# Kernel tuning notes

Measured on AMD Instinct MI355X. Metric: run time of the kernel, lower is better.

Reference implementation:

```python
import jax, jax.numpy as jnp
import numpy as np
from jax import lax

K = 4
H = 1024
IN = 512
OUT = 8192
T = 128
B = 32


def setup_inputs() -> dict:
    key = jax.random.key(0)
    ks = jax.random.split(key, 5)
    return {
        "X": jax.random.normal(ks[0], (T, B, IN), dtype=jnp.float32),
        "Wxh_w": jax.random.normal(ks[1], (H, IN), dtype=jnp.float32) * 0.02,
        "Wxh_b": jax.random.normal(ks[2], (H,), dtype=jnp.float32) * 0.02,
        "Whh_w": jax.random.normal(ks[3], (H, (K - 1) * H), dtype=jnp.float32) * 0.02,
        "Wmo_w": jax.random.normal(ks[4], (OUT, K * H), dtype=jnp.float32) * 0.02,
    }


def reference(X, Wxh_w, Wxh_b, Whh_w, Wmo_w):
    batch = X.shape[1]
    # history stack hs: [K-1, B, H], hs[0] = oldest, hs[-1] = newest
    hs0 = jnp.zeros((K - 1, batch, H), dtype=X.dtype)

    def step(hs, x_t):
        # concat reversed(h_prevs): newest block first -> [B, (K-1)*H]
        h_cat = hs[::-1].transpose(1, 0, 2).reshape(batch, (K - 1) * H)
        h_t = jax.nn.selu(x_t @ Wxh_w.T + Wxh_b + h_cat @ Whh_w.T)  # [B, H]
        h_out = jnp.concatenate([h_t, h_cat], axis=1)  # [B, K*H]
        out_t = h_out @ Wmo_w.T  # [B, OUT]
        new_hs = jnp.concatenate([hs[1:], h_t[None]], axis=0)
        # truncated BPTT: detach the (new) oldest hidden
        new_hs = new_hs.at[0].set(lax.stop_gradient(new_hs[0]))
        return new_hs, out_t

    _, outs = lax.scan(step, hs0, X)
    return outs  # [T, B, OUT]
```

## Files before the change

kernel.cpp:

```cpp
#include <hip/hip_runtime.h>
#include <hip/hip_bf16.h>

#define T_STEPS 128
#define BATCH   32
#define IN_DIM  512
#define H_DIM   1024
#define OUT_DIM 8192
#define KH      3072
#define NWG     128
#define SLOT_E  32768
#define NSLOT   131

typedef __attribute__((ext_vector_type(8))) short short8;
typedef __attribute__((ext_vector_type(4))) float f32x4;

__device__ __forceinline__ unsigned short bf16_rne(float f) {
  unsigned u = __float_as_uint(f);
  unsigned r = (u + 0x7FFFu + ((u >> 16) & 1u)) >> 16;
  return (unsigned short)r;
}

__device__ __forceinline__ void gload_lds16(const void* g, void* l) {
  __builtin_amdgcn_global_load_lds(
      (const __attribute__((address_space(1))) void*)g,
      (__attribute__((address_space(3))) void*)l, 16, 0, 0);
}

__global__ __launch_bounds__(256) void convert_kernel(
    const float* __restrict__ src, unsigned short* __restrict__ dst, int n4) {
  int i = blockIdx.x * blockDim.x + threadIdx.x;
  const int stride = gridDim.x * blockDim.x;
  for (; i < n4; i += stride) {
    float4 v = ((const float4*)src)[i];
    ushort4 o;
    o.x = bf16_rne(v.x); o.y = bf16_rne(v.y);
    o.z = bf16_rne(v.z); o.w = bf16_rne(v.w);
    ((ushort4*)dst)[i] = o;
  }
}

__global__ __launch_bounds__(256) void pre_kernel(
    const float* __restrict__ X, const float* __restrict__ Wxh,
    const float* __restrict__ bias, float* __restrict__ preT) {
  __shared__ float xs[32][260];
  const int tid = threadIdx.x;
  const int t  = blockIdx.x >> 4;
  const int jb = blockIdx.x & 15;
  const int b  = tid & 31;
  const int jg = tid >> 5;
  float acc[8];
  #pragma unroll
  for (int i = 0; i < 8; ++i) acc[i] = 0.f;

  for (int kc = 0; kc < 2; ++kc) {
    __syncthreads();
    #pragma unroll
    for (int v = tid; v < 2048; v += 256) {
      int br = v >> 6, i4 = v & 63;
      float4 x4 = *(const float4*)(X + (size_t)t*(BATCH*IN_DIM) + (size_t)br*IN_DIM + kc*256 + i4*4);
      *(float4*)&xs[br][i4*4] = x4;
    }
    __syncthreads();
    for (int i = 0; i < 256; i += 4) {
      const int k = kc*256 + i;
      float4 xv = *(const float4*)&xs[b][i];
      #pragma unroll
      for (int jj = 0; jj < 8; ++jj) {
        const int j = jb*64 + jg + jj*8;
        float4 w4 = *(const float4*)(Wxh + (size_t)j*IN_DIM + k);
        acc[jj] += xv.x*w4.x + xv.y*w4.y + xv.z*w4.z + xv.w*w4.w;
      }
    }
  }
  #pragma unroll
  for (int jj = 0; jj < 8; ++jj) {
    const int j = jb*64 + jg + jj*8;
    preT[(size_t)t*(H_DIM*BATCH) + (size_t)j*BATCH + b] = acc[jj] + bias[j];
  }
}

template<int RN, int RD1, int RD2>
__device__ __forceinline__ void do_step(
    const int t, const int tid, const int wg, const int j0,
    const int lane, const int wv,
    const short8* __restrict__ wf, const short8* __restrict__ hi8,
    const short8* __restrict__ lo8, const float* __restrict__ preT,
    unsigned short* __restrict__ hHi, unsigned short* __restrict__ hLo,
    int* __restrict__ grp, int* __restrict__ rootcnt, int* __restrict__ rootrep,
    short8 (&Rh0)[3][4], short8 (&Rh1)[3][4],
    short8 (&Rl0)[3][4], short8 (&Rl1)[3][4],
    float (&red)[8][16][33],
    unsigned short (&hpk_hi)[32][8], unsigned short (&hpk_lo)[32][8]) {
  f32x4 a0h = {}, a0l = {}, a1h = {}, a1l = {};

  #pragma unroll
  for (int i = 0; i < 4; ++i) {
    const int ks = 32 + wv*4 + i;
    const short8 af = wf[ks*64 + lane];
    a0h = __builtin_amdgcn_mfma_f32_16x16x32_bf16(af, Rh0[RD1][i], a0h, 0, 0, 0);
    a1h = __builtin_amdgcn_mfma_f32_16x16x32_bf16(af, Rh1[RD1][i], a1h, 0, 0, 0);
    a0l = __builtin_amdgcn_mfma_f32_16x16x32_bf16(af, Rl0[RD1][i], a0l, 0, 0, 0);
    a1l = __builtin_amdgcn_mfma_f32_16x16x32_bf16(af, Rl1[RD1][i], a1l, 0, 0, 0);
  }
  #pragma unroll
  for (int i = 0; i < 4; ++i) {
    const int ks = 64 + wv*4 + i;
    const short8 af = wf[ks*64 + lane];
    a0h = __builtin_amdgcn_mfma_f32_16x16x32_bf16(af, Rh0[RD2][i], a0h, 0, 0, 0);
    a1h = __builtin_amdgcn_mfma_f32_16x16x32_bf16(af, Rh1[RD2][i], a1h, 0, 0, 0);
    a0l = __builtin_amdgcn_mfma_f32_16x16x32_bf16(af, Rl0[RD2][i], a0l, 0, 0, 0);
    a1l = __builtin_amdgcn_mfma_f32_16x16x32_bf16(af, Rl1[RD2][i], a1l, 0, 0, 0);
  }

  float upre = 0.f;
  if (tid < 256)
    upre = preT[(size_t)t*(H_DIM*BATCH) + (size_t)(j0 + (tid >> 5))*BATCH + (tid & 31)];

  if (t > 0) {
    if (tid == 0) {
      while (!__hip_atomic_load(&rootrep[(((t-1) << 3) + (wg & 7)) << 4],
                                __ATOMIC_RELAXED, __HIP_MEMORY_SCOPE_AGENT))
        __builtin_amdgcn_s_sleep(2);
    }
    __syncthreads();
    asm volatile("" ::: "memory");
  }

  {
    const size_t sb = (size_t)(128 - t) * 4096;
    #pragma unroll
    for (int i = 0; i < 4; ++i) {
      const int ks = wv*4 + i;
      const size_t bidx = sb + (size_t)ks*128 + (size_t)(lane >> 4)*32 + (lane & 15);
      Rh0[RN][i] = hi8[bidx];
      Rh1[RN][i] = hi8[bidx + 16];
      Rl0[RN][i] = lo8[bidx];
      Rl1[RN][i] = lo8[bidx + 16];
    }
  }
  #pragma unroll
  for (int i = 0; i < 4; ++i) {
    const int ks = wv*4 + i;
    const short8 af = wf[ks*64 + lane];
    a0h = __builtin_amdgcn_mfma_f32_16x16x32_bf16(af, Rh0[RN][i], a0h, 0, 0, 0);
    a1h = __builtin_amdgcn_mfma_f32_16x16x32_bf16(af, Rh1[RN][i], a1h, 0, 0, 0);
    a0l = __builtin_amdgcn_mfma_f32_16x16x32_bf16(af, Rl0[RN][i], a0l, 0, 0, 0);
    a1l = __builtin_amdgcn_mfma_f32_16x16x32_bf16(af, Rl1[RN][i], a1l, 0, 0, 0);
  }

  const f32x4 s0 = a0h + a0l;
  const f32x4 s1 = a1h + a1l;
  const int rr = (lane >> 4) * 4, cc = lane & 15;
  #pragma unroll
  for (int q = 0; q < 4; ++q) {
    red[wv][rr + q][cc]      = s0[q];
    red[wv][rr + q][16 + cc] = s1[q];
  }
  __syncthreads();

  if (tid < 256) {
    const int jj = tid >> 5, b = tid & 31;
    float u = upre;
    #pragma unroll
    for (int w = 0; w < 8; ++w)
      u += red[w][jj][b] + red[w][jj + 8][b];
    const float h = u > 0.f ? 1.0507009873554805f*u
                            : (1.0507009873554805f*1.6732632423543772f)*expm1f(u);
    const unsigned short hh = bf16_rne(h);
    hpk_hi[b][jj] = hh;
    hpk_lo[b][jj] = bf16_rne(h - __uint_as_float((unsigned)hh << 16));
  }
  __syncthreads();

  if (tid < 32) {
    const int b = tid;
    const size_t base = (size_t)(127 - t)*SLOT_E + (size_t)(j0 >> 3)*256 + (size_t)b*8;
    const unsigned long long h0 = *(const unsigned long long*)&hpk_hi[b][0];
    const unsigned long long h1 = *(const unsigned long long*)&hpk_hi[b][4];
    const unsigned long long l0 = *(const unsigned long long*)&hpk_lo[b][0];
    const unsigned long long l1 = *(const unsigned long long*)&hpk_lo[b][4];
    __hip_atomic_store((unsigned long long*)(hHi + base),     h0, __ATOMIC_RELAXED, __HIP_MEMORY_SCOPE_AGENT);
    __hip_atomic_store((unsigned long long*)(hHi + base) + 1, h1, __ATOMIC_RELAXED, __HIP_MEMORY_SCOPE_AGENT);
    __hip_atomic_store((unsigned long long*)(hLo + base),     l0, __ATOMIC_RELAXED, __HIP_MEMORY_SCOPE_AGENT);
    __hip_atomic_store((unsigned long long*)(hLo + base) + 1, l1, __ATOMIC_RELAXED, __HIP_MEMORY_SCOPE_AGENT);
    if (t < T_STEPS - 1) {
      asm volatile("s_waitcnt vmcnt(0)" ::: "memory");
      if (tid == 0) {
        const int g = wg >> 3;
        if (__hip_atomic_fetch_add(&grp[((t << 4) + g) << 4], 1, __ATOMIC_RELAXED, __HIP_MEMORY_SCOPE_AGENT) == 7) {
          if (__hip_atomic_fetch_add(&rootcnt[t << 4], 1, __ATOMIC_RELAXED, __HIP_MEMORY_SCOPE_AGENT) == 15) {
            #pragma unroll
            for (int r = 0; r < 8; ++r)
              __hip_atomic_store(&rootrep[((t << 3) + r) << 4], 1,
                                 __ATOMIC_RELAXED, __HIP_MEMORY_SCOPE_AGENT);
          }
        }
      }
    }
  }
}

__global__ __launch_bounds__(512, 2) void recur_kernel(
    const float* __restrict__ Whh, const float* __restrict__ preT,
    unsigned short* __restrict__ hHi, unsigned short* __restrict__ hLo,
    int* __restrict__ grp, int* __restrict__ rootcnt, int* __restrict__ rootrep) {
  __shared__ __align__(16) unsigned short w_lds[96*64*8];
  __shared__ float red[8][16][33];
  __shared__ __align__(16) unsigned short hpk_hi[32][8];
  __shared__ __align__(16) unsigned short hpk_lo[32][8];
  const int tid  = threadIdx.x;
  const int wg   = blockIdx.x;
  const int j0   = wg * 8;
  const int lane = tid & 63;
  const int wv   = tid >> 6;

  for (int s = tid; s < 6144; s += 512) {
    const int ks = s >> 6, l = s & 63;
    const int r = l & 15;
    const int j = j0 + (r & 7);
    const int part = r >> 3;
    const int kb = ks*32 + (l >> 4)*8;
    const float* wp = Whh + (size_t)j*KH + kb;
    unsigned short tmp[8];
    #pragma unroll
    for (int i = 0; i < 8; ++i) {
      const float f = wp[i];
      unsigned short v = bf16_rne(f);
      if (part) v = bf16_rne(f - __uint_as_float((unsigned)v << 16));
      tmp[i] = v;
    }
    *(short8*)&w_lds[s*8] = *(short8*)tmp;
  }
  __syncthreads();

  const short8* wf  = (const short8*)w_lds;
  const short8* hi8 = (const short8*)hHi;
  const short8* lo8 = (const short8*)hLo;

  short8 Rh0[3][4], Rh1[3][4], Rl0[3][4], Rl1[3][4];
  const short8 z8 = {};
  #pragma unroll
  for (int r = 1; r < 3; ++r)
    #pragma unroll
    for (int i = 0; i < 4; ++i) {
      Rh0[r][i] = z8; Rh1[r][i] = z8; Rl0[r][i] = z8; Rl1[r][i] = z8;
    }

  for (int t3 = 0; t3 < 126; t3 += 3) {
    do_step<0,2,1>(t3,   tid, wg, j0, lane, wv, wf, hi8, lo8, preT, hHi, hLo,
                   grp, rootcnt, rootrep, Rh0, Rh1, Rl0, Rl1, red, hpk_hi, hpk_lo);
    do_step<1,0,2>(t3+1, tid, wg, j0, lane, wv, wf, hi8, lo8, preT, hHi, hLo,
                   grp, rootcnt, rootrep, Rh0, Rh1, Rl0, Rl1, red, hpk_hi, hpk_lo);
    do_step<2,1,0>(t3+2, tid, wg, j0, lane, wv, wf, hi8, lo8, preT, hHi, hLo,
                   grp, rootcnt, rootrep, Rh0, Rh1, Rl0, Rl1, red, hpk_hi, hpk_lo);
  }
  do_step<0,2,1>(126, tid, wg, j0, lane, wv, wf, hi8, lo8, preT, hHi, hLo,
                 grp, rootcnt, rootrep, Rh0, Rh1, Rl0, Rl1, red, hpk_hi, hpk_lo);
  do_step<1,0,2>(127, tid, wg, j0, lane, wv, wf, hi8, lo8, preT, hHi, hLo,
                 grp, rootcnt, rootrep, Rh0, Rh1, Rl0, Rl1, red, hpk_hi, hpk_lo);
}

__global__ __launch_bounds__(256) void gemm_kernel(
    const unsigned short* __restrict__ Ah, const unsigned short* __restrict__ Bm,
    float* __restrict__ C) {
  __shared__ __align__(16) unsigned short lA[2][4096];
  __shared__ __align__(16) unsigned short lB[2][4096];
  const int tid = threadIdx.x;
  const int wg = blockIdx.x;
  const int mb = wg & 31;
  const int nb = wg >> 5;
  const int lane = tid & 63;
  const int wv = tid >> 6;
  const int wm = wv >> 1, wn = wv & 1;
  const int lrow = lane & 15, lhalf = lane >> 4;
  const int rowB0 = tid >> 2, qB = tid & 3;
  f32x4 acc[4][4] = {};

#define STAGE(buf, kt) do {                                                    \
    _Pragma("unroll")                                                          \
    for (int it = 0; it < 2; ++it) {                                           \
      const int idxA = it*4 + wv;                                              \
      const int tA = mb*4 + (idxA >> 1);                                       \
      gload_lds16(Ah + (size_t)(127 - tA)*SLOT_E + (size_t)(kt)*1024           \
                     + (idxA & 1)*512 + (size_t)lane*8,                        \
                  &lA[buf][idxA*512]);                                         \
      const int rB = it*64 + rowB0;                                            \
      const int qs = qB ^ ((rB ^ (rB >> 2)) & 3);                              \
      gload_lds16(Bm + (size_t)(nb*128 + rB)*4096 + (size_t)(kt)*32 + qs*8,    \
                  &lB[buf][(tid & 192)*8 + it*2048]);                          \
    } } while (0)

  STAGE(0, 0);
  for (int kt = 0; kt < 128; ++kt) {
    const int cur = kt & 1;
    if (kt < 127) {
      STAGE(cur ^ 1, kt + 1);
      asm volatile("s_waitcnt vmcnt(4)" ::: "memory");
    } else {
      asm volatile("s_waitcnt vmcnt(0)" ::: "memory");
    }
    __syncthreads();
    short8 af[4], bf[4];
    #pragma unroll
    for (int mi = 0; mi < 4; ++mi) {
      const int tg = wm*2 + (mi >> 1);
      af[mi] = *(const short8*)&lA[cur][tg*1024 + lhalf*256 + (lrow + (mi & 1)*16)*8];
    }
    #pragma unroll
    for (int ni = 0; ni < 4; ++ni) {
      const int r = wn*64 + ni*16 + lrow;
      const int qs = lhalf ^ ((r ^ (r >> 2)) & 3);
      bf[ni] = *(const short8*)&lB[cur][r*32 + qs*8];
    }
    #pragma unroll
    for (int mi = 0; mi < 4; ++mi)
      #pragma unroll
      for (int ni = 0; ni < 4; ++ni)
        acc[mi][ni] = __builtin_amdgcn_mfma_f32_16x16x32_bf16(af[mi], bf[ni], acc[mi][ni], 0, 0, 0);
    __syncthreads();
  }
#undef STAGE

  const int orow0 = mb*128 + wm*64 + lhalf*4;
  const int ocol0 = nb*128 + wn*64 + lrow;
  #pragma unroll
  for (int mi = 0; mi < 4; ++mi)
    #pragma unroll
    for (int ni = 0; ni < 4; ++ni)
      #pragma unroll
      for (int q = 0; q < 4; ++q)
        __builtin_nontemporal_store(acc[mi][ni][q],
            &C[(size_t)(orow0 + mi*16 + q)*OUT_DIM + ocol0 + ni*16]);
}

extern "C" void kernel_launch(void* const* d_in, const int* in_sizes, int n_in,
                              void* d_out, int out_size, void* d_ws, size_t ws_size,
                              hipStream_t stream) {
  (void)in_sizes; (void)n_in; (void)out_size; (void)ws_size;
  const float* X   = (const float*)d_in[0];
  const float* Wxh = (const float*)d_in[1];
  const float* Wxb = (const float*)d_in[2];
  const float* Whh = (const float*)d_in[3];
  const float* Wmo = (const float*)d_in[4];
  float* out = (float*)d_out;
  char* ws = (char*)d_ws;

  const size_t OFF_PRET = 0;
  const size_t OFF_HHI  = OFF_PRET + (size_t)T_STEPS*H_DIM*BATCH*4;
  const size_t OFF_HLO  = OFF_HHI + (size_t)NSLOT*SLOT_E*2;
  const size_t OFF_GRP  = OFF_HLO + (size_t)NSLOT*SLOT_E*2;
  const size_t OFF_RCNT = OFF_GRP + (size_t)T_STEPS*16*64;
  const size_t OFF_RREP = OFF_RCNT + (size_t)T_STEPS*64;
  const size_t OFF_W16  = OFF_RREP + (size_t)T_STEPS*8*64;

  float* preT = (float*)(ws + OFF_PRET);
  unsigned short* hHi = (unsigned short*)(ws + OFF_HHI);
  unsigned short* hLo = (unsigned short*)(ws + OFF_HLO);
  int* grp     = (int*)(ws + OFF_GRP);
  int* rootcnt = (int*)(ws + OFF_RCNT);
  int* rootrep = (int*)(ws + OFF_RREP);
  unsigned short* Wmo16 = (unsigned short*)(ws + OFF_W16);

  hipMemsetAsync(hHi + (size_t)128*SLOT_E, 0, (size_t)3*SLOT_E*2, stream);
  hipMemsetAsync(hLo + (size_t)128*SLOT_E, 0, (size_t)3*SLOT_E*2, stream);
  hipMemsetAsync(grp, 0, (size_t)T_STEPS*16*64 + (size_t)T_STEPS*64
                        + (size_t)T_STEPS*8*64, stream);

  convert_kernel<<<2048, 256, 0, stream>>>(Wmo, Wmo16, (int)((size_t)OUT_DIM*4096/4));
  pre_kernel<<<2048, 256, 0, stream>>>(X, Wxh, Wxb, preT);
  recur_kernel<<<NWG, 512, 0, stream>>>(Whh, preT, hHi, hLo, grp, rootcnt, rootrep);
  gemm_kernel<<<2048, 256, 0, stream>>>(hHi, Wmo16, out);
}
```

Before: 1.138 ms.

## Replace output GEMM with 256x256-tile, 8-wave, 8-phase pipelined kernel

Rewrites the final output GEMM. It now uses 256x256 output tiles per workgroup with 512 threads, 128 KB of dynamic LDS holding double-buffered 64-wide K slices, and an eight-phase schedule that interleaves quarter-tile global-to-LDS staging with MFMA work. It also adds s_setprio around the MFMA bursts and a grouped block-to-tile mapping. The aim is to raise arithmetic intensity and overlap loads with compute. The cost is higher register and LDS pressure, and a fragile hand-written barrier and vmcnt schedule.

```diff
diff --git a/kernel.cpp b/kernel.cpp
--- a/kernel.cpp
+++ b/kernel.cpp
@@ -260,77 +260,121 @@
                  grp, rootcnt, rootrep, Rh0, Rh1, Rl0, Rl1, red, hpk_hi, hpk_lo);
 }
 
-__global__ __launch_bounds__(256) void gemm_kernel(
+__global__ __launch_bounds__(512, 2) void gemm256_kernel(
     const unsigned short* __restrict__ Ah, const unsigned short* __restrict__ Bm,
     float* __restrict__ C) {
-  __shared__ __align__(16) unsigned short lA[2][4096];
-  __shared__ __align__(16) unsigned short lB[2][4096];
+  extern __shared__ char smem[];
   const int tid = threadIdx.x;
   const int wg = blockIdx.x;
-  const int mb = wg & 31;
-  const int nb = wg >> 5;
+  const int x = wg & 7;
+  const int c = wg >> 3;
+  const int mb = c & 15;
+  const int nb = x*4 + (c >> 4);
   const int lane = tid & 63;
   const int wv = tid >> 6;
-  const int wm = wv >> 1, wn = wv & 1;
+  const int wm = wv >> 2;
+  const int wn = wv & 3;
   const int lrow = lane & 15, lhalf = lane >> 4;
-  const int rowB0 = tid >> 2, qB = tid & 3;
-  f32x4 acc[4][4] = {};
-
-#define STAGE(buf, kt) do {                                                    \
+  const int srow = tid & 127;
+  const int ss0 = tid >> 7;
+  int tA[2], bA[2];
+  #pragma unroll
+  for (int h = 0; h < 2; ++h) {
+    const int m = mb*256 + h*128 + srow;
+    tA[h] = m >> 5; bA[h] = m & 31;
+  }
+
+#define STAGE_A(HALF, BUF, KT) do {                                            \
     _Pragma("unroll")                                                          \
-    for (int it = 0; it < 2; ++it) {                                           \
-      const int idxA = it*4 + wv;                                              \
-      const int tA = mb*4 + (idxA >> 1);                                       \
-      gload_lds16(Ah + (size_t)(127 - tA)*SLOT_E + (size_t)(kt)*1024           \
-                     + (idxA & 1)*512 + (size_t)lane*8,                        \
-                  &lA[buf][idxA*512]);                                         \
-      const int rB = it*64 + rowB0;                                            \
-      const int qs = qB ^ ((rB ^ (rB >> 2)) & 3);                              \
-      gload_lds16(Bm + (size_t)(nb*128 + rB)*4096 + (size_t)(kt)*32 + qs*8,    \
-                  &lB[buf][(tid & 192)*8 + it*2048]);                          \
+    for (int u = 0; u < 2; ++u) {                                              \
+      const int s_ = u*4 + ss0;                                                \
+      gload_lds16(Ah + (size_t)(127 - tA[HALF])*SLOT_E                         \
+                     + (size_t)((KT)*8 + s_)*256 + bA[HALF]*8,                 \
+                  smem + (BUF)*65536 + (HALF)*16384 + u*8192 + tid*16);        \
     } } while (0)
 
-  STAGE(0, 0);
-  for (int kt = 0; kt < 128; ++kt) {
-    const int cur = kt & 1;
-    if (kt < 127) {
-      STAGE(cur ^ 1, kt + 1);
-      asm volatile("s_waitcnt vmcnt(4)" ::: "memory");
-    } else {
-      asm volatile("s_waitcnt vmcnt(0)" ::: "memory");
-    }
-    __syncthreads();
-    short8 af[4], bf[4];
-    #pragma unroll
-    for (int mi = 0; mi < 4; ++mi) {
-      const int tg = wm*2 + (mi >> 1);
-      af[mi] = *(const short8*)&lA[cur][tg*1024 + lhalf*256 + (lrow + (mi & 1)*16)*8];
-    }
-    #pragma unroll
-    for (int ni = 0; ni < 4; ++ni) {
-      const int r = wn*64 + ni*16 + lrow;
-      const int qs = lhalf ^ ((r ^ (r >> 2)) & 3);
-      bf[ni] = *(const short8*)&lB[cur][r*32 + qs*8];
-    }
-    #pragma unroll
-    for (int mi = 0; mi < 4; ++mi)
-      #pragma unroll
-      for (int ni = 0; ni < 4; ++ni)
-        acc[mi][ni] = __builtin_amdgcn_mfma_f32_16x16x32_bf16(af[mi], bf[ni], acc[mi][ni], 0, 0, 0);
-    __syncthreads();
-  }
-#undef STAGE
-
-  const int orow0 = mb*128 + wm*64 + lhalf*4;
-  const int ocol0 = nb*128 + wn*64 + lrow;
-  #pragma unroll
-  for (int mi = 0; mi < 4; ++mi)
-    #pragma unroll
-    for (int ni = 0; ni < 4; ++ni)
+#define STAGE_B(HALF, BUF, KT) do {                                            \
+    _Pragma("unroll")                                                          \
+    for (int u = 0; u < 2; ++u) {                                              \
+      const int s_ = u*4 + ss0;                                                \
+      gload_lds16(Bm + (size_t)(nb*256 + (HALF)*128 + srow)*4096               \
+                     + (size_t)(KT)*64 + s_*8,                                 \
+                  smem + (BUF)*65536 + 32768 + (HALF)*16384 + u*8192 + tid*16);\
+    } } while (0)
+
+  short8 aF[4][2], bF[2][2];
+  f32x4 acc[8][4] = {};
+
+#define PHASE(BUF, MH, NH, RDA, RDB, STAGE_STMT, DO_VM) do {                   \
+    if (RDA) {                                                                 \
+      _Pragma("unroll")                                                        \
+      for (int mi = 0; mi < 4; ++mi)                                           \
+        _Pragma("unroll")                                                      \
+        for (int kk = 0; kk < 2; ++kk)                                         \
+          aF[mi][kk] = *(const short8*)(smem + (BUF)*65536 + wm*16384          \
+              + (kk*4 + lhalf)*2048 + ((MH)*64 + mi*16 + lrow)*16);            \
+    }                                                                          \
+    if (RDB) {                                                                 \
+      _Pragma("unroll")                                                        \
+      for (int ni = 0; ni < 2; ++ni)                                           \
+        _Pragma("unroll")                                                      \
+        for (int kk = 0; kk < 2; ++kk)                                         \
+          bF[ni][kk] = *(const short8*)(smem + (BUF)*65536 + 32768             \
+              + (wn >> 1)*16384 + (kk*4 + lhalf)*2048                          \
+              + ((wn & 1)*64 + (NH)*32 + ni*16 + lrow)*16);                    \
+    }                                                                          \
+    STAGE_STMT;                                                                \
+    __builtin_amdgcn_s_barrier();                                              \
+    __builtin_amdgcn_s_setprio(1);                                             \
+    _Pragma("unroll")                                                          \
+    for (int mi = 0; mi < 4; ++mi)                                             \
+      _Pragma("unroll")                                                        \
+      for (int ni = 0; ni < 2; ++ni) {                                         \
+        acc[(MH)*4+mi][(NH)*2+ni] = __builtin_amdgcn_mfma_f32_16x16x32_bf16(   \
+            aF[mi][0], bF[ni][0], acc[(MH)*4+mi][(NH)*2+ni], 0, 0, 0);         \
+        acc[(MH)*4+mi][(NH)*2+ni] = __builtin_amdgcn_mfma_f32_16x16x32_bf16(   \
+            aF[mi][1], bF[ni][1], acc[(MH)*4+mi][(NH)*2+ni], 0, 0, 0);         \
+      }                                                                        \
+    __builtin_amdgcn_s_setprio(0);                                             \
+    if (DO_VM) asm volatile("s_waitcnt vmcnt(2)" ::: "memory");                \
+    __builtin_amdgcn_s_barrier();                                              \
+  } while (0)
+
+  STAGE_A(0, 0, 0);
+  STAGE_B(0, 0, 0);
+  STAGE_B(1, 0, 0);
+  STAGE_A(1, 0, 0);
+  STAGE_A(0, 1, 1);
+  asm volatile("s_waitcnt vmcnt(2)" ::: "memory");
+  __builtin_amdgcn_s_barrier();
+
+  for (int j = 0; j < 32; ++j) {
+    const int k1 = 2*j + 1;
+    const int k2 = (2*j + 2 < 64) ? 2*j + 2 : 63;
+    const int k3 = (2*j + 3 < 64) ? 2*j + 3 : 63;
+    PHASE(0, 0, 0, 1, 1, STAGE_B(0, 1, k1), 0);
+    PHASE(0, 0, 1, 0, 1, STAGE_B(1, 1, k1), 0);
+    PHASE(0, 1, 1, 1, 0, STAGE_A(1, 1, k1), 0);
+    PHASE(0, 1, 0, 0, 1, STAGE_A(0, 0, k2), 1);
+    PHASE(1, 0, 0, 1, 1, STAGE_B(0, 0, k2), 0);
+    PHASE(1, 0, 1, 0, 1, STAGE_B(1, 0, k2), 0);
+    PHASE(1, 1, 1, 1, 0, STAGE_A(1, 0, k2), 0);
+    PHASE(1, 1, 0, 0, 1, STAGE_A(0, 1, k3), 1);
+  }
+#undef PHASE
+#undef STAGE_A
+#undef STAGE_B
+
+  const int orow0 = mb*256 + wm*128 + lhalf*4;
+  const int ocol0 = nb*256 + wn*64 + lrow;
+  #pragma unroll
+  for (int m_ = 0; m_ < 8; ++m_)
+    #pragma unroll
+    for (int n_ = 0; n_ < 4; ++n_)
       #pragma unroll
       for (int q = 0; q < 4; ++q)
-        __builtin_nontemporal_store(acc[mi][ni][q],
-            &C[(size_t)(orow0 + mi*16 + q)*OUT_DIM + ocol0 + ni*16]);
+        __builtin_nontemporal_store(acc[m_][n_][q],
+            &C[(size_t)(orow0 + m_*16 + q)*OUT_DIM + ocol0 + n_*16]);
 }
 
 extern "C" void kernel_launch(void* const* d_in, const int* in_sizes, int n_in,
@@ -361,6 +405,9 @@
   int* rootrep = (int*)(ws + OFF_RREP);
   unsigned short* Wmo16 = (unsigned short*)(ws + OFF_W16);
 
+  (void)hipFuncSetAttribute(reinterpret_cast<const void*>(gemm256_kernel),
+                            hipFuncAttributeMaxDynamicSharedMemorySize, 131072);
+
   hipMemsetAsync(hHi + (size_t)128*SLOT_E, 0, (size_t)3*SLOT_E*2, stream);
   hipMemsetAsync(hLo + (size_t)128*SLOT_E, 0, (size_t)3*SLOT_E*2, stream);
   hipMemsetAsync(grp, 0, (size_t)T_STEPS*16*64 + (size_t)T_STEPS*64
@@ -369,5 +416,5 @@
   convert_kernel<<<2048, 256, 0, stream>>>(Wmo, Wmo16, (int)((size_t)OUT_DIM*4096/4));
   pre_kernel<<<2048, 256, 0, stream>>>(X, Wxh, Wxb, preT);
   recur_kernel<<<NWG, 512, 0, stream>>>(Whh, preT, hHi, hLo, grp, rootcnt, rootrep);
-  gemm_kernel<<<2048, 256, 0, stream>>>(hHi, Wmo16, out);
-}
+  gemm256_kernel<<<512, 512, 131072, stream>>>(hHi, Wmo16, out);
+}
```

After: 1.060 ms. -6.9%, faster.
